# Kernel tuning notes

Measured on AMD Instinct MI355X. Metric: run time of the kernel, lower is better.

## Reference

```python
import jax, jax.numpy as jnp
import numpy as np

BN_EPS = 1e-5


def setup_inputs() -> dict:
    key = jax.random.key(0)
    ks = jax.random.split(key, 8)
    b, c, h, w, k = 8, 512, 128, 128, 64
    x = jax.random.normal(ks[0], (b, c, h, w), dtype=jnp.float32)
    # 1x1 conv weights stored as 2D matrices (out_ch, in_ch)
    conv1_w = jax.random.normal(ks[1], (c, c), dtype=jnp.float32) * np.sqrt(2.0 / c)
    conv1_b = jnp.zeros((c,), dtype=jnp.float32)
    lin0_w = jax.random.normal(ks[2], (k, c), dtype=jnp.float32) * np.sqrt(2.0 / k)
    lin1_w = jnp.transpose(lin0_w)  # tied init: linear_1.weight = linear_0.weight.permute(1,0,2)
    conv2_w = jax.random.normal(ks[3], (c, c), dtype=jnp.float32) * np.sqrt(2.0 / c)
    bn_gamma = jnp.ones((c,), dtype=jnp.float32)
    bn_beta = jnp.zeros((c,), dtype=jnp.float32)
    return {"x": x, "conv1_w": conv1_w, "conv1_b": conv1_b, "lin0_w": lin0_w,
            "lin1_w": lin1_w, "conv2_w": conv2_w, "bn_gamma": bn_gamma, "bn_beta": bn_beta}


def reference(x, conv1_w, conv1_b, lin0_w, lin1_w, conv2_w, bn_gamma, bn_beta):
    b, c, h, w = x.shape
    idn = x
    # conv1: 1x1 conv == channel GEMM
    y = jnp.einsum('oc,bchw->bohw', conv1_w, x) + conv1_b[None, :, None, None]
    y = y.reshape(b, c, h * w)                       # [b, c, n]
    attn = jnp.einsum('kc,bcn->bkn', lin0_w, y)      # [b, k, n]
    attn = jax.nn.softmax(attn, axis=-1)             # softmax over spatial n
    attn = attn / (1e-9 + attn.sum(axis=1, keepdims=True))  # L1 renorm over k
    y = jnp.einsum('ck,bkn->bcn', lin1_w, attn)      # [b, c, n]
    y = y.reshape(b, c, h, w)
    # conv2 (1x1, no bias) + BatchNorm2d (training mode: batch stats, biased var)
    y = jnp.einsum('oc,bchw->bohw', conv2_w, y)
    mean = y.mean(axis=(0, 2, 3))
    var = y.var(axis=(0, 2, 3))
    y = (y - mean[None, :, None, None]) * jax.lax.rsqrt(var + BN_EPS)[None, :, None, None]
    y = y * bn_gamma[None, :, None, None] + bn_beta[None, :, None, None]
    return jax.nn.relu(y + idn)
```

## Files before the change

kernel.cpp:

```cpp
#include <hip/hip_runtime.h>

#define C_DIM 512
#define K_DIM 64
#define B_DIM 8
#define N_DIM 16384
#define BN_CNT (B_DIM * N_DIM)
#define BN_EPS 1e-5f
#define TILE_N 128
#define ES_STRIDE 132
#define K4_BLOCKS 256

__global__ __launch_bounds__(256) void k_prep(
    const float* __restrict__ conv1_w, const float* __restrict__ conv1_b,
    const float* __restrict__ lin0_w, const float* __restrict__ lin1_w,
    const float* __restrict__ conv2_w,
    float* __restrict__ W0t, float* __restrict__ W2p, float* __restrict__ b0) {
  int id = blockIdx.x * 256 + threadIdx.x;
  if (id < C_DIM * K_DIM) {
    int c = id / K_DIM, k = id % K_DIM;
    float acc = 0.f;
    for (int cp = 0; cp < C_DIM; ++cp)
      acc = fmaf(lin0_w[k * C_DIM + cp], conv1_w[cp * C_DIM + c], acc);
    W0t[id] = acc;
  } else if (id < 2 * C_DIM * K_DIM) {
    int id2 = id - C_DIM * K_DIM;
    int o = id2 / K_DIM, k = id2 % K_DIM;
    float acc = 0.f;
    for (int cc = 0; cc < C_DIM; ++cc)
      acc = fmaf(conv2_w[o * C_DIM + cc], lin1_w[cc * K_DIM + k], acc);
    W2p[id2] = acc;
  } else if (id < 2 * C_DIM * K_DIM + K_DIM) {
    int k = id - 2 * C_DIM * K_DIM;
    float acc = 0.f;
    for (int cp = 0; cp < C_DIM; ++cp)
      acc = fmaf(lin0_w[k * C_DIM + cp], conv1_b[cp], acc);
    b0[k] = acc;
  }
}

__global__ __launch_bounds__(256) void k_attn_logits(
    const float* __restrict__ x, const float* __restrict__ W0t,
    const float* __restrict__ b0, float* __restrict__ A) {
  int pix = blockIdx.x * 256 + threadIdx.x;
  int b = pix >> 14;
  int n = pix & 16383;
  const float* xp = x + (size_t)b * C_DIM * N_DIM + n;
  float acc[K_DIM];
#pragma unroll
  for (int k = 0; k < K_DIM; ++k) acc[k] = b0[k];
  for (int c = 0; c < C_DIM; ++c) {
    float xv = xp[(size_t)c * N_DIM];
    const float* w = W0t + c * K_DIM;
#pragma unroll
    for (int k = 0; k < K_DIM; ++k) acc[k] = fmaf(w[k], xv, acc[k]);
  }
  float* ap = A + (size_t)b * K_DIM * N_DIM + n;
#pragma unroll
  for (int k = 0; k < K_DIM; ++k) ap[(size_t)k * N_DIM] = acc[k];
}

__global__ __launch_bounds__(256) void k_rowstats(
    const float* __restrict__ A, float* __restrict__ rowmax, float* __restrict__ rowsum) {
  int row = blockIdx.x;
  const float4* ap = (const float4*)(A + (size_t)row * N_DIM);
  float m = -1e30f, s = 0.f;
  for (int i = threadIdx.x; i < N_DIM / 4; i += 256) {
    float4 v = ap[i];
    float lm = fmaxf(fmaxf(v.x, v.y), fmaxf(v.z, v.w));
    float nm = fmaxf(m, lm);
    s = s * __expf(m - nm) + __expf(v.x - nm) + __expf(v.y - nm) +
        __expf(v.z - nm) + __expf(v.w - nm);
    m = nm;
  }
  __shared__ float sm[256], ss[256];
  sm[threadIdx.x] = m; ss[threadIdx.x] = s;
  __syncthreads();
  for (int off = 128; off >= 1; off >>= 1) {
    if (threadIdx.x < off) {
      float m1 = sm[threadIdx.x], s1 = ss[threadIdx.x];
      float m2 = sm[threadIdx.x + off], s2 = ss[threadIdx.x + off];
      float nm = fmaxf(m1, m2);
      sm[threadIdx.x] = nm;
      ss[threadIdx.x] = s1 * __expf(m1 - nm) + s2 * __expf(m2 - nm);
    }
    __syncthreads();
  }
  if (threadIdx.x == 0) { rowmax[row] = sm[0]; rowsum[row] = ss[0]; }
}

__global__ __launch_bounds__(256) void k_softmax_renorm(
    float* __restrict__ A, const float* __restrict__ rowmax,
    const float* __restrict__ rowsum,
    float* __restrict__ meanApart, float* __restrict__ Cpart) {
  __shared__ float es[K_DIM][ES_STRIDE];
  __shared__ float csinv[TILE_N];
  __shared__ float rm[K_DIM], rsi[K_DIM];
  int t = threadIdx.x;
  float cacc[16];
#pragma unroll
  for (int i = 0; i < 16; ++i) cacc[i] = 0.f;
  float macc = 0.f;
  int k1 = t >> 2;
  int k2lo = t & 3;

  int krow0 = t >> 5;
  int n4 = (t & 31) * 4;

  for (int tile = blockIdx.x; tile < B_DIM * (N_DIM / TILE_N); tile += gridDim.x) {
    int b = tile / (N_DIM / TILE_N);
    int n0 = (tile % (N_DIM / TILE_N)) * TILE_N;
    if (t < K_DIM) {
      rm[t] = rowmax[b * K_DIM + t];
      rsi[t] = 1.f / rowsum[b * K_DIM + t];
    }
    __syncthreads();
    float* ab = A + (size_t)b * K_DIM * N_DIM + n0;
#pragma unroll
    for (int kk = 0; kk < 8; ++kk) {
      int krow = kk * 8 + krow0;
      float4 v = *(const float4*)(ab + (size_t)krow * N_DIM + n4);
      float mm = rm[krow], si = rsi[krow];
      v.x = __expf(v.x - mm) * si;
      v.y = __expf(v.y - mm) * si;
      v.z = __expf(v.z - mm) * si;
      v.w = __expf(v.w - mm) * si;
      *(float4*)&es[krow][n4] = v;
    }
    __syncthreads();
    if (t < TILE_N) {
      float cs = 0.f;
#pragma unroll
      for (int k = 0; k < K_DIM; ++k) cs += es[k][t];
      csinv[t] = 1.f / (1e-9f + cs);
    }
    __syncthreads();
#pragma unroll
    for (int kk = 0; kk < 8; ++kk) {
      int krow = kk * 8 + krow0;
      float4 v = *(float4*)&es[krow][n4];
      float4 ci = *(const float4*)&csinv[n4];
      v.x *= ci.x; v.y *= ci.y; v.z *= ci.z; v.w *= ci.w;
      *(float4*)&es[krow][n4] = v;
      *(float4*)(ab + (size_t)krow * N_DIM + n4) = v;
    }
    __syncthreads();
    if (t < K_DIM) {
      float s = 0.f;
#pragma unroll 8
      for (int n = 0; n < TILE_N; ++n) s += es[t][n];
      macc += s;
    }
#pragma unroll 4
    for (int q = 0; q < TILE_N / 4; ++q) {
      float4 v1 = *(const float4*)&es[k1][q * 4];
#pragma unroll
      for (int j = 0; j < 16; ++j) {
        float4 v2 = *(const float4*)&es[k2lo + 4 * j][q * 4];
        cacc[j] = fmaf(v1.x, v2.x, cacc[j]);
        cacc[j] = fmaf(v1.y, v2.y, cacc[j]);
        cacc[j] = fmaf(v1.z, v2.z, cacc[j]);
        cacc[j] = fmaf(v1.w, v2.w, cacc[j]);
      }
    }
    __syncthreads();
  }
  if (t < K_DIM) meanApart[blockIdx.x * K_DIM + t] = macc;
  float* cp = Cpart + (size_t)blockIdx.x * (K_DIM * K_DIM) + k1 * K_DIM + k2lo;
#pragma unroll
  for (int j = 0; j < 16; ++j) cp[4 * j] = cacc[j];
}

__global__ __launch_bounds__(256) void k_reduce_parts(
    const float* __restrict__ Cpart, const float* __restrict__ meanApart,
    float* __restrict__ Csum, float* __restrict__ meanA) {
  int j = blockIdx.x * 256 + threadIdx.x;
  if (j < K_DIM * K_DIM) {
    float s = 0.f;
    for (int p = 0; p < K4_BLOCKS; ++p) s += Cpart[(size_t)p * K_DIM * K_DIM + j];
    Csum[j] = s;
  } else if (j < K_DIM * K_DIM + K_DIM) {
    int k = j - K_DIM * K_DIM;
    float s = 0.f;
    for (int p = 0; p < K4_BLOCKS; ++p) s += meanApart[p * K_DIM + k];
    meanA[k] = s;
  }
}

__global__ __launch_bounds__(64) void k_bn_coeffs(
    const float* __restrict__ W2p, const float* __restrict__ Csum,
    const float* __restrict__ meanA,
    const float* __restrict__ gamma, const float* __restrict__ beta,
    float* __restrict__ scale, float* __restrict__ shift) {
  __shared__ float Cs[K_DIM][K_DIM];
  __shared__ float mAs[K_DIM];
  int t = threadIdx.x;
  for (int i = t; i < K_DIM * K_DIM; i += 64) ((float*)Cs)[i] = Csum[i];
  mAs[t] = meanA[t];
  __syncthreads();
  int o = blockIdx.x * 64 + t;
  float w[K_DIM];
#pragma unroll
  for (int k = 0; k < K_DIM; ++k) w[k] = W2p[o * K_DIM + k];
  const float invBN = 1.f / (float)BN_CNT;
  float m = 0.f;
#pragma unroll
  for (int k = 0; k < K_DIM; ++k) m = fmaf(w[k], mAs[k], m);
  m *= invBN;
  float q = 0.f;
  for (int k = 0; k < K_DIM; ++k) {
    float tk = 0.f;
#pragma unroll
    for (int kp = 0; kp < K_DIM; ++kp) tk = fmaf(w[kp], Cs[kp][k], tk);
    q = fmaf(tk, w[k], q);
  }
  q *= invBN;
  float var = q - m * m;
  float sc = gamma[o] * rsqrtf(var + BN_EPS);
  scale[o] = sc;
  shift[o] = beta[o] - m * sc;
}

__global__ __launch_bounds__(256) void k_output(
    const float* __restrict__ x, const float* __restrict__ A,
    const float* __restrict__ W2p, const float* __restrict__ scale,
    const float* __restrict__ shift, float* __restrict__ out) {
  int pix = blockIdx.x * 256 + threadIdx.x;
  int b = pix >> 14;
  int n = pix & 16383;
  const float* ap = A + (size_t)b * K_DIM * N_DIM + n;
  float at[K_DIM];
#pragma unroll
  for (int k = 0; k < K_DIM; ++k) at[k] = ap[(size_t)k * N_DIM];
  const float* xp = x + (size_t)b * C_DIM * N_DIM + n;
  float* op = out + (size_t)b * C_DIM * N_DIM + n;
  for (int o = 0; o < C_DIM; ++o) {
    const float* w = W2p + o * K_DIM;
    float xv = xp[(size_t)o * N_DIM];
    float a0 = 0.f, a1 = 0.f, a2 = 0.f, a3 = 0.f;
#pragma unroll
    for (int k = 0; k < K_DIM; k += 4) {
      a0 = fmaf(w[k], at[k], a0);
      a1 = fmaf(w[k + 1], at[k + 1], a1);
      a2 = fmaf(w[k + 2], at[k + 2], a2);
      a3 = fmaf(w[k + 3], at[k + 3], a3);
    }
    float y = (a0 + a1) + (a2 + a3);
    y = fmaf(y, scale[o], shift[o]) + xv;
    op[(size_t)o * N_DIM] = fmaxf(y, 0.f);
  }
}

extern "C" void kernel_launch(void* const* d_in, const int* in_sizes, int n_in,
                              void* d_out, int out_size, void* d_ws, size_t ws_size,
                              hipStream_t stream) {
  (void)in_sizes; (void)n_in; (void)out_size; (void)ws_size;
  const float* x       = (const float*)d_in[0];
  const float* conv1_w = (const float*)d_in[1];
  const float* conv1_b = (const float*)d_in[2];
  const float* lin0_w  = (const float*)d_in[3];
  const float* lin1_w  = (const float*)d_in[4];
  const float* conv2_w = (const float*)d_in[5];
  const float* gamma   = (const float*)d_in[6];
  const float* beta    = (const float*)d_in[7];
  float* out = (float*)d_out;
  float* ws  = (float*)d_ws;

  float* A         = ws;
  float* W0t       = A + (size_t)B_DIM * K_DIM * N_DIM;
  float* W2p       = W0t + C_DIM * K_DIM;
  float* b0        = W2p + C_DIM * K_DIM;
  float* rowmax    = b0 + K_DIM;
  float* rowsum    = rowmax + B_DIM * K_DIM;
  float* meanApart = rowsum + B_DIM * K_DIM;
  float* Cpart     = meanApart + K4_BLOCKS * K_DIM;
  float* meanA     = Cpart + (size_t)K4_BLOCKS * K_DIM * K_DIM;
  float* Csum      = meanA + K_DIM;
  float* scale     = Csum + K_DIM * K_DIM;
  float* shift     = scale + C_DIM;

  k_prep<<<(2 * C_DIM * K_DIM + K_DIM + 255) / 256, 256, 0, stream>>>(
      conv1_w, conv1_b, lin0_w, lin1_w, conv2_w, W0t, W2p, b0);
  k_attn_logits<<<(B_DIM * N_DIM) / 256, 256, 0, stream>>>(x, W0t, b0, A);
  k_rowstats<<<B_DIM * K_DIM, 256, 0, stream>>>(A, rowmax, rowsum);
  k_softmax_renorm<<<K4_BLOCKS, 256, 0, stream>>>(A, rowmax, rowsum, meanApart, Cpart);
  k_reduce_parts<<<(K_DIM * K_DIM + K_DIM + 255) / 256, 256, 0, stream>>>(
      Cpart, meanApart, Csum, meanA);
  k_bn_coeffs<<<C_DIM / 64, 64, 0, stream>>>(W2p, Csum, meanA, gamma, beta, scale, shift);
  k_output<<<(B_DIM * N_DIM) / 256, 256, 0, stream>>>(x, A, W2p, scale, shift, out);
}
```

Measured before the change: 1.300 ms.

## Split output over channel chunks, batch loads, size softmax partials from workspace

The output kernel gets a second grid dimension over 128-channel chunks, which adds parallelism, and batches 8 residual loads and stores per iteration. The logits kernel batches 8 input-channel loads before its FMA loop. The prep kernel remaps thread indices so the conv1_w reads coalesce, and the softmax-stats kernel now launches 256 or 512 partial blocks depending on workspace size. The risk is that each output chunk block reloads the 64 attention values, which adds A traffic, and that unknown parts of the softmax kernel may assume a fixed block count.

```diff
diff --git a/kernel.cpp b/kernel.cpp
--- a/kernel.cpp
+++ b/kernel.cpp
@@ -8,7 +8,8 @@
 #define BN_EPS 1e-5f
 #define TILE_N 128
 #define ES_STRIDE 132
-#define K4_BLOCKS 256
+#define OCHUNK 128
+#define K4_MAX 512
 
 __global__ __launch_bounds__(256) void k_prep(
     const float* __restrict__ conv1_w, const float* __restrict__ conv1_b,
@@ -17,15 +18,18 @@
     float* __restrict__ W0t, float* __restrict__ W2p, float* __restrict__ b0) {
   int id = blockIdx.x * 256 + threadIdx.x;
   if (id < C_DIM * K_DIM) {
-    int c = id / K_DIM, k = id % K_DIM;
+    int k = id >> 9;
+    int c = id & 511;
     float acc = 0.f;
+#pragma unroll 4
     for (int cp = 0; cp < C_DIM; ++cp)
       acc = fmaf(lin0_w[k * C_DIM + cp], conv1_w[cp * C_DIM + c], acc);
-    W0t[id] = acc;
+    W0t[c * K_DIM + k] = acc;
   } else if (id < 2 * C_DIM * K_DIM) {
     int id2 = id - C_DIM * K_DIM;
-    int o = id2 / K_DIM, k = id2 % K_DIM;
+    int o = id2 >> 6, k = id2 & 63;
     float acc = 0.f;
+#pragma unroll 4
     for (int cc = 0; cc < C_DIM; ++cc)
       acc = fmaf(conv2_w[o * C_DIM + cc], lin1_w[cc * K_DIM + k], acc);
     W2p[id2] = acc;
@@ -48,11 +52,16 @@
   float acc[K_DIM];
 #pragma unroll
   for (int k = 0; k < K_DIM; ++k) acc[k] = b0[k];
-  for (int c = 0; c < C_DIM; ++c) {
-    float xv = xp[(size_t)c * N_DIM];
-    const float* w = W0t + c * K_DIM;
-#pragma unroll
-    for (int k = 0; k < K_DIM; ++k) acc[k] = fmaf(w[k], xv, acc[k]);
+  for (int c = 0; c < C_DIM; c += 8) {
+    float xv[8];
+#pragma unroll
+    for (int j = 0; j < 8; ++j) xv[j] = xp[(size_t)(c + j) * N_DIM];
+#pragma unroll
+    for (int j = 0; j < 8; ++j) {
+      const float* w = W0t + (c + j) * K_DIM;
+#pragma unroll
+      for (int k = 0; k < K_DIM; ++k) acc[k] = fmaf(w[k], xv[j], acc[k]);
+    }
   }
   float* ap = A + (size_t)b * K_DIM * N_DIM + n;
 #pragma unroll
@@ -172,16 +181,16 @@
 
 __global__ __launch_bounds__(256) void k_reduce_parts(
     const float* __restrict__ Cpart, const float* __restrict__ meanApart,
-    float* __restrict__ Csum, float* __restrict__ meanA) {
+    float* __restrict__ Csum, float* __restrict__ meanA, int P) {
   int j = blockIdx.x * 256 + threadIdx.x;
   if (j < K_DIM * K_DIM) {
     float s = 0.f;
-    for (int p = 0; p < K4_BLOCKS; ++p) s += Cpart[(size_t)p * K_DIM * K_DIM + j];
+    for (int p = 0; p < P; ++p) s += Cpart[(size_t)p * K_DIM * K_DIM + j];
     Csum[j] = s;
   } else if (j < K_DIM * K_DIM + K_DIM) {
     int k = j - K_DIM * K_DIM;
     float s = 0.f;
-    for (int p = 0; p < K4_BLOCKS; ++p) s += meanApart[p * K_DIM + k];
+    for (int p = 0; p < P; ++p) s += meanApart[p * K_DIM + k];
     meanA[k] = s;
   }
 }
@@ -227,33 +236,42 @@
   int pix = blockIdx.x * 256 + threadIdx.x;
   int b = pix >> 14;
   int n = pix & 16383;
+  int o0 = blockIdx.y * OCHUNK;
   const float* ap = A + (size_t)b * K_DIM * N_DIM + n;
   float at[K_DIM];
 #pragma unroll
   for (int k = 0; k < K_DIM; ++k) at[k] = ap[(size_t)k * N_DIM];
   const float* xp = x + (size_t)b * C_DIM * N_DIM + n;
   float* op = out + (size_t)b * C_DIM * N_DIM + n;
-  for (int o = 0; o < C_DIM; ++o) {
-    const float* w = W2p + o * K_DIM;
-    float xv = xp[(size_t)o * N_DIM];
-    float a0 = 0.f, a1 = 0.f, a2 = 0.f, a3 = 0.f;
-#pragma unroll
-    for (int k = 0; k < K_DIM; k += 4) {
-      a0 = fmaf(w[k], at[k], a0);
-      a1 = fmaf(w[k + 1], at[k + 1], a1);
-      a2 = fmaf(w[k + 2], at[k + 2], a2);
-      a3 = fmaf(w[k + 3], at[k + 3], a3);
-    }
-    float y = (a0 + a1) + (a2 + a3);
-    y = fmaf(y, scale[o], shift[o]) + xv;
-    op[(size_t)o * N_DIM] = fmaxf(y, 0.f);
+  for (int o = o0; o < o0 + OCHUNK; o += 8) {
+    float xv[8];
+#pragma unroll
+    for (int j = 0; j < 8; ++j) xv[j] = xp[(size_t)(o + j) * N_DIM];
+    float y[8];
+#pragma unroll
+    for (int j = 0; j < 8; ++j) {
+      const float* w = W2p + (o + j) * K_DIM;
+      float a0 = 0.f, a1 = 0.f, a2 = 0.f, a3 = 0.f;
+#pragma unroll
+      for (int k = 0; k < K_DIM; k += 4) {
+        a0 = fmaf(w[k], at[k], a0);
+        a1 = fmaf(w[k + 1], at[k + 1], a1);
+        a2 = fmaf(w[k + 2], at[k + 2], a2);
+        a3 = fmaf(w[k + 3], at[k + 3], a3);
+      }
+      float yy = (a0 + a1) + (a2 + a3);
+      y[j] = fmaf(yy, scale[o + j], shift[o + j]) + xv[j];
+    }
+#pragma unroll
+    for (int j = 0; j < 8; ++j)
+      op[(size_t)(o + j) * N_DIM] = fmaxf(y[j], 0.f);
   }
 }
 
 extern "C" void kernel_launch(void* const* d_in, const int* in_sizes, int n_in,
                               void* d_out, int out_size, void* d_ws, size_t ws_size,
                               hipStream_t stream) {
-  (void)in_sizes; (void)n_in; (void)out_size; (void)ws_size;
+  (void)in_sizes; (void)n_in; (void)out_size;
   const float* x       = (const float*)d_in[0];
   const float* conv1_w = (const float*)d_in[1];
   const float* conv1_b = (const float*)d_in[2];
@@ -265,26 +283,33 @@
   float* out = (float*)d_out;
   float* ws  = (float*)d_ws;
 
-  float* A         = ws;
-  float* W0t       = A + (size_t)B_DIM * K_DIM * N_DIM;
-  float* W2p       = W0t + C_DIM * K_DIM;
-  float* b0        = W2p + C_DIM * K_DIM;
-  float* rowmax    = b0 + K_DIM;
-  float* rowsum    = rowmax + B_DIM * K_DIM;
-  float* meanApart = rowsum + B_DIM * K_DIM;
-  float* Cpart     = meanApart + K4_BLOCKS * K_DIM;
-  float* meanA     = Cpart + (size_t)K4_BLOCKS * K_DIM * K_DIM;
-  float* Csum      = meanA + K_DIM;
-  float* scale     = Csum + K_DIM * K_DIM;
-  float* shift     = scale + C_DIM;
+  float* A      = ws;
+  float* W0t    = A + (size_t)B_DIM * K_DIM * N_DIM;
+  float* W2p    = W0t + C_DIM * K_DIM;
+  float* b0     = W2p + C_DIM * K_DIM;
+  float* rowmax = b0 + K_DIM;
+  float* rowsum = rowmax + B_DIM * K_DIM;
+  float* meanA  = rowsum + B_DIM * K_DIM;
+  float* Csum   = meanA + K_DIM;
+  float* scale  = Csum + K_DIM * K_DIM;
+  float* shift  = scale + C_DIM;
+  float* meanApart = shift + C_DIM;
+  size_t used = (size_t)(meanApart - ws);
+  size_t avail = ws_size / sizeof(float) - used;
+  int P = (int)(avail / (K_DIM * K_DIM + K_DIM));
+  if (P > K4_MAX) P = K4_MAX;
+  if (P > 256) P = 512 <= P ? 512 : 256;
+  if (P < 1) P = 1;
+  float* Cpart = meanApart + (size_t)P * K_DIM;
 
   k_prep<<<(2 * C_DIM * K_DIM + K_DIM + 255) / 256, 256, 0, stream>>>(
       conv1_w, conv1_b, lin0_w, lin1_w, conv2_w, W0t, W2p, b0);
   k_attn_logits<<<(B_DIM * N_DIM) / 256, 256, 0, stream>>>(x, W0t, b0, A);
   k_rowstats<<<B_DIM * K_DIM, 256, 0, stream>>>(A, rowmax, rowsum);
-  k_softmax_renorm<<<K4_BLOCKS, 256, 0, stream>>>(A, rowmax, rowsum, meanApart, Cpart);
+  k_softmax_renorm<<<P, 256, 0, stream>>>(A, rowmax, rowsum, meanApart, Cpart);
   k_reduce_parts<<<(K_DIM * K_DIM + K_DIM + 255) / 256, 256, 0, stream>>>(
-      Cpart, meanApart, Csum, meanA);
+      Cpart, meanApart, Csum, meanA, P);
   k_bn_coeffs<<<C_DIM / 64, 64, 0, stream>>>(W2p, Csum, meanA, gamma, beta, scale, shift);
-  k_output<<<(B_DIM * N_DIM) / 256, 256, 0, stream>>>(x, A, W2p, scale, shift, out);
-}
+  dim3 og((B_DIM * N_DIM) / 256, C_DIM / OCHUNK);
+  k_output<<<og, 256, 0, stream>>>(x, A, W2p, scale, shift, out);
+}
```

New measurement: 1.058 ms. -18.6%, faster.
